# Performance work log

Measured on AMD Instinct MI355X. Metric: run time of the kernel, lower is better.

## Reference

```python
import jax, jax.numpy as jnp
import numpy as np
import math

B, S, D, H, L, K = 4, 2048, 256, 8, 2, 3  # batch, seq, dim, heads, MTA layers, conv kernel
HS = D // H
EPS = 1e-6


def layer_norm(x, g, b):
    m = jnp.mean(x, axis=-1, keepdims=True)
    v = jnp.mean((x - m) ** 2, axis=-1, keepdims=True)
    return (x - m) * jax.lax.rsqrt(v + EPS) * g + b


def temporal_encoder(x, W, b):
    # x: [B,S,D]; W: [L,K,D,D] (WIO), b: [L,D]. Stack of kernel-3 'SAME' Conv1d, GELU between.
    for i in range(L):
        x = jax.lax.conv_general_dilated(
            x, W[i], window_strides=(1,), padding=[(1, 1)],
            dimension_numbers=("NWC", "WIO", "NWC")) + b[i]
        if i < L - 1:
            x = jax.nn.gelu(x)
    return x


def setup_inputs() -> dict:
    key = jax.random.key(0)
    ks = jax.random.split(key, 10)
    w = lambda k, shape: jax.random.normal(k, shape, jnp.float32) * 0.02
    return {
        "x": jax.random.normal(ks[0], (B, S, D), jnp.float32),
        "ln1_g": jnp.ones((D,), jnp.float32), "ln1_b": jnp.zeros((D,), jnp.float32),
        "Wq": w(ks[1], (L, K, D, D)), "bq": jnp.zeros((L, D), jnp.float32),
        "Wk": w(ks[2], (L, K, D, D)), "bk": jnp.zeros((L, D), jnp.float32),
        "Wv": w(ks[3], (L, K, D, D)), "bv": jnp.zeros((L, D), jnp.float32),
        "ln2_g": jnp.ones((D,), jnp.float32), "ln2_b": jnp.zeros((D,), jnp.float32),
        "Wo1": w(ks[4], (D, D)), "bo1": jnp.zeros((D,), jnp.float32),
        "Wo2": w(ks[5], (D, D)), "bo2": jnp.zeros((D,), jnp.float32),
        "mask": jax.random.randint(ks[6], (B, S), 0, 2).astype(jnp.int32),
    }


def reference(x, ln1_g, ln1_b, Wq, bq, Wk, bk, Wv, bv, ln2_g, ln2_b, Wo1, bo1, Wo2, bo2, mask):
    b_, s_ = x.shape[0], x.shape[1]
    h = layer_norm(x, ln1_g, ln1_b)
    q = temporal_encoder(h, Wq, bq).reshape(b_, s_, H, HS)
    k = temporal_encoder(h, Wk, bk).reshape(b_, s_, H, HS)
    v = temporal_encoder(h, Wv, bv).reshape(b_, s_, H, HS)
    # attention scores [B,H,S,S]
    scores = jnp.einsum("bqhd,bkhd->bhqk", q, k) / math.sqrt(HS)
    m = mask[:, None, None, :].astype(scores.dtype)  # [B,1,1,S]
    scores = scores + (1.0 - m) * (-1e30)
    probs = jax.nn.softmax(scores, axis=-1)
    attn = jnp.einsum("bhqk,bkhd->bqhd", probs, v).reshape(b_, s_, D)
    residual = x + attn  # dropout p=0
    o = layer_norm(residual, ln2_g, ln2_b)
    o = jax.nn.gelu(o @ Wo1 + bo1)  # 1x1 Conv1D == per-token linear
    o = o @ Wo2 + bo2 + residual
    return o
```

## Files before the change

kernel.cpp:

```cpp
#include <hip/hip_runtime.h>
#include <hip/hip_bf16.h>
#include <math.h>

#define BB 4
#define SS 2048
#define DD 256
#define HH 8
#define HSZ 32

typedef __attribute__((ext_vector_type(8))) short short8;
typedef __attribute__((ext_vector_type(4))) float f32x4;

__device__ __forceinline__ void gload_lds16(const void* g, void* l) {
    __builtin_amdgcn_global_load_lds((const unsigned int*)g, (unsigned int*)l,
                                     16, 0, 0);
}

__device__ __forceinline__ float exp2_hw(float x) {
    float r;
    asm("v_exp_f32 %0, %1" : "=v"(r) : "v"(x));
    return r;
}

__device__ __forceinline__ unsigned int perm_pack(float a, float b, unsigned int sel) {
    unsigned int r;
    asm("v_perm_b32 %0, %1, %2, %3"
        : "=v"(r)
        : "v"(__float_as_uint(b)), "v"(__float_as_uint(a)), "s"(sel));
    return r;
}

__device__ __forceinline__ float gelu_f(float x) {
    float x3 = x * x * x;
    float z = 0.7978845608028654f * fmaf(0.044715f, x3, x);
    float e = __expf(2.0f * z);
    float t = 1.0f - 2.0f / (e + 1.0f);
    return 0.5f * x * (1.0f + t);
}

__device__ __forceinline__ unsigned short f2bf(float f) {
    unsigned int u = __float_as_uint(f);
    u = (u + 0x7fffu + ((u >> 16) & 1u)) >> 16;
    return (unsigned short)u;
}

template<bool HASRES>
__device__ __forceinline__ void ln_wave_body(
    int t, int lane,
    const float* __restrict__ x, const float* __restrict__ addin,
    const float* __restrict__ g, const float* __restrict__ bvec,
    float* __restrict__ resid_out, unsigned short* __restrict__ oln_bf)
{
    const int base = t * DD + lane * 4;
    float4 v4 = *(const float4*)&x[base];
    if (HASRES) {
        float4 a4 = *(const float4*)&addin[base];
        v4.x += a4.x; v4.y += a4.y; v4.z += a4.z; v4.w += a4.w;
        *(float4*)&resid_out[base] = v4;
    }
    float s = (v4.x + v4.y) + (v4.z + v4.w);
    #pragma unroll
    for (int o = 1; o < 64; o <<= 1) s += __shfl_xor(s, o);
    float mean = s * (1.0f / 256.0f);
    float dx = v4.x - mean, dy = v4.y - mean, dz = v4.z - mean, dw = v4.w - mean;
    float q = (dx * dx + dy * dy) + (dz * dz + dw * dw);
    #pragma unroll
    for (int o = 1; o < 64; o <<= 1) q += __shfl_xor(q, o);
    float r = rsqrtf(q * (1.0f / 256.0f) + 1e-6f);
    const float4 g4 = *(const float4*)&g[lane * 4];
    const float4 b4 = *(const float4*)&bvec[lane * 4];
    ushort4 o4;
    o4.x = f2bf(dx * r * g4.x + b4.x);
    o4.y = f2bf(dy * r * g4.y + b4.y);
    o4.z = f2bf(dz * r * g4.z + b4.z);
    o4.w = f2bf(dw * r * g4.w + b4.w);
    *(ushort4*)&oln_bf[base] = o4;
}

__global__ __launch_bounds__(256) void prep_kernel(
    const float* __restrict__ Wq, const float* __restrict__ Wk,
    const float* __restrict__ Wv, const float* __restrict__ Wo1,
    const float* __restrict__ Wo2, unsigned short* __restrict__ wt,
    const float* __restrict__ x, const float* __restrict__ ln1g,
    const float* __restrict__ ln1b, unsigned short* __restrict__ h_bf,
    const int* __restrict__ mask, float* __restrict__ maskf)
{
    if (blockIdx.x < 1280) {
        const int WCp = 3 * DD * DD;
        const int WMp = DD * DD;
        const float* src; unsigned short* dst; int rel;
        int i = blockIdx.x;
        if (i < 1152) {
            int seg = i / 192; rel = i % 192;
            src = seg == 0 ? Wq : seg == 1 ? Wq + WCp : seg == 2 ? Wk :
                  seg == 3 ? Wk + WCp : seg == 4 ? Wv : Wv + WCp;
            dst = wt + (size_t)seg * WCp;
        } else {
            int j = i - 1152; int seg = j / 64; rel = j % 64;
            src = seg == 0 ? Wo1 : Wo2;
            dst = wt + (size_t)6 * WCp + (size_t)seg * WMp;
        }
        __shared__ unsigned short t[32][33];
        const int tx = threadIdx.x & 31, ty = threadIdx.x >> 5;
        const int r0 = (rel / 8) * 32, c0 = (rel % 8) * 32;
        #pragma unroll
        for (int j = 0; j < 32; j += 8)
            t[ty + j][tx] = f2bf(src[(r0 + ty + j) * 256 + c0 + tx]);
        __syncthreads();
        #pragma unroll
        for (int j = 0; j < 32; j += 8) {
            unsigned int och = (unsigned int)(c0 + ty + j);
            unsigned int k   = (unsigned int)(r0 + tx);
            unsigned int u   = och * 32u + (k & 31u);
            u ^= ((u >> 6) & 7u) << 3;
            dst[(size_t)(k >> 5) * 8192 + u] = t[tx][ty + j];
        }
    } else if (blockIdx.x < 3328) {
        const int wv = threadIdx.x >> 6, lane = threadIdx.x & 63;
        ln_wave_body<false>((blockIdx.x - 1280) * 4 + wv, lane,
                            x, nullptr, ln1g, ln1b, nullptr, h_bf);
    } else {
        const float M_ON  = -8.0f * 1.4426950408889634f;
        const float M_OFF = -1.442695e30f;
        int i = (blockIdx.x - 3328) * 1024 + threadIdx.x * 4;
        int4 m4 = *(const int4*)&mask[i];
        float4 f4;
        f4.x = m4.x ? M_ON : M_OFF;
        f4.y = m4.y ? M_ON : M_OFF;
        f4.z = m4.z ? M_ON : M_OFF;
        f4.w = m4.w ? M_ON : M_OFF;
        *(float4*)&maskf[i] = f4;
    }
}

__global__ __launch_bounds__(256, 3) void convdual_kernel(
    const unsigned short* __restrict__ in,
    const unsigned short* __restrict__ W0a, const unsigned short* __restrict__ W0b,
    const unsigned short* __restrict__ W0c,
    const unsigned short* __restrict__ W1a, const unsigned short* __restrict__ W1b,
    const unsigned short* __restrict__ W1c,
    const float* __restrict__ ba, const float* __restrict__ bb,
    const float* __restrict__ bc,
    unsigned short* __restrict__ oQ, unsigned short* __restrict__ oK,
    unsigned short* __restrict__ oV, int S)
{
    constexpr int LDW = 264;
    __shared__ __align__(16) unsigned short stage[36 * LDW];
    __shared__ __align__(16) unsigned short wbuf[2][8192];

    unsigned short* const inter = stage;

    const int set = blockIdx.x % 3;
    const int tile = blockIdx.x / 3;
    const unsigned short* W0 = set == 0 ? W0a : (set == 1 ? W0b : W0c);
    const unsigned short* W1 = set == 0 ? W1a : (set == 1 ? W1b : W1c);
    const float* bias         = set == 0 ? ba  : (set == 1 ? bb  : bc);
    unsigned short* outp      = set == 0 ? oQ  : (set == 1 ? oK  : oV);

    const int tid = threadIdx.x;
    const int lane = tid & 63, wv = tid >> 6;
    const int lm = lane & 15, lq = lane >> 4;
    const int tpb = S / 32;
    const int b = tile / tpb;
    const int s0 = (tile % tpb) * 32;
    const int NC = S / 32;
    const int c = s0 >> 5;

    for (int i = tid; i < 36 * 32; i += 256) {
        int r = i >> 5, c8 = (i & 31) << 3;
        int s = s0 + r - 2;
        int4 val = make_int4(0, 0, 0, 0);
        if (s >= 0 && s < S)
            val = *(const int4*)&in[(size_t)(b * S + s) * 256 + c8];
        *(int4*)&stage[r * LDW + c8] = val;
    }

    const int n0 = wv * 64;

    const int wq = wv * 4096;
    const char* w0p = (const char*)W0 + wq + lane * 16;
    const char* w1p = (const char*)W1 + wq + lane * 16;
    char* const wb0 = (char*)wbuf;

    unsigned int boff[4];
    #pragma unroll
    for (int nt = 0; nt < 4; ++nt) {
        unsigned int och = (unsigned int)(n0 + nt * 16 + lm);
        unsigned int R = och * 64u + (unsigned int)lq * 16u;
        boff[nt] = R ^ (((R >> 7) & 7u) << 4);
    }

    __syncthreads();

    {
        f32x4 acc[3][4];
        #pragma unroll
        for (int mt = 0; mt < 3; ++mt)
            #pragma unroll
            for (int nt = 0; nt < 4; ++nt) acc[mt][nt] = (f32x4){0.f, 0.f, 0.f, 0.f};

        #pragma unroll
        for (int j = 0; j < 4; ++j) gload_lds16(w0p + j * 1024,         wb0 + wq + j * 1024);
        #pragma unroll
        for (int j = 0; j < 4; ++j) gload_lds16(w0p + 16384 + j * 1024, wb0 + 16384 + wq + j * 1024);

        short8 a0c, a1c, a2c;
        {
            const int icc0 = lq * 8;
            int r20 = 32 + lm; r20 = r20 > 35 ? 35 : r20;
            a0c = *(const short8*)&stage[lm * LDW + icc0];
            a1c = *(const short8*)&stage[(16 + lm) * LDW + icc0];
            a2c = *(const short8*)&stage[r20 * LDW + icc0];
        }

        asm volatile("s_waitcnt vmcnt(4)" ::: "memory");
        __builtin_amdgcn_sched_barrier(0);
        short8 bfc[4];
        #pragma unroll
        for (int nt = 0; nt < 4; ++nt)
            bfc[nt] = *(const short8*)(wb0 + boff[nt]);

        #pragma unroll
        for (int it = 0; it < 24; ++it) {
            asm volatile("s_waitcnt lgkmcnt(0)" ::: "memory");
            __builtin_amdgcn_sched_barrier(0);
            if (it + 2 < 24) {
                char* ld = wb0 + ((it & 1) << 14) + wq;
                const int soff = (it + 2) * 16384;
                #pragma unroll
                for (int j = 0; j < 4; ++j)
                    gload_lds16(w0p + soff + j * 1024, ld + j * 1024);
            }
            __builtin_amdgcn_sched_barrier(0);
            if (it < 22)       { asm volatile("s_waitcnt vmcnt(4)" ::: "memory"); }
            else if (it == 22) { asm volatile("s_waitcnt vmcnt(0)" ::: "memory"); }
            __builtin_amdgcn_sched_barrier(0);

            short8 bfn[4];
            short8 a0n, a1n, a2n;
            if (it + 1 < 24) {
                const char* wb = wb0 + (((it + 1) & 1) << 14);
                #pragma unroll
                for (int nt = 0; nt < 4; ++nt)
                    bfn[nt] = *(const short8*)(wb + boff[nt]);
                const int kk = (it + 1) >> 3;
                const int icc = ((it + 1) & 7) * 32 + lq * 8;
                int r2 = kk + 32 + lm; r2 = r2 > 35 ? 35 : r2;
                a0n = *(const short8*)&stage[(kk + lm) * LDW + icc];
                a1n = *(const short8*)&stage[(kk + 16 + lm) * LDW + icc];
                a2n = *(const short8*)&stage[r2 * LDW + icc];
            }
            __builtin_amdgcn_s_setprio(1);
            #pragma unroll
            for (int nt = 0; nt < 4; ++nt) {
                acc[0][nt] = __builtin_amdgcn_mfma_f32_16x16x32_bf16(a0c, bfc[nt], acc[0][nt], 0, 0, 0);
                acc[1][nt] = __builtin_amdgcn_mfma_f32_16x16x32_bf16(a1c, bfc[nt], acc[1][nt], 0, 0, 0);
                acc[2][nt] = __builtin_amdgcn_mfma_f32_16x16x32_bf16(a2c, bfc[nt], acc[2][nt], 0, 0, 0);
            }
            __builtin_amdgcn_s_setprio(0);
            if (it + 1 < 24) {
                #pragma unroll
                for (int nt = 0; nt < 4; ++nt) bfc[nt] = bfn[nt];
                a0c = a0n; a1c = a1n; a2c = a2n;
            }
        }

        __syncthreads();

        #pragma unroll
        for (int j = 0; j < 4; ++j) gload_lds16(w1p + j * 1024,         wb0 + wq + j * 1024);
        #pragma unroll
        for (int j = 0; j < 4; ++j) gload_lds16(w1p + 16384 + j * 1024, wb0 + 16384 + wq + j * 1024);

        #pragma unroll
        for (int mt = 0; mt < 3; ++mt)
            #pragma unroll
            for (int nt = 0; nt < 4; ++nt) {
                int ch = n0 + nt * 16 + lm;
                float bv = bias[ch];
                #pragma unroll
                for (int r = 0; r < 4; ++r) {
                    int j = mt * 16 + lq * 4 + r;
                    if (j < 34) {
                        int token = s0 - 1 + j;
                        unsigned short v = (token >= 0 && token < S)
                            ? f2bf(gelu_f(acc[mt][nt][r] + bv)) : (unsigned short)0;
                        inter[j * LDW + ch] = v;
                    }
                }
            }
    }
    __syncthreads();

    f32x4 acc2[2][4];
    #pragma unroll
    for (int mt = 0; mt < 2; ++mt)
        #pragma unroll
        for (int nt = 0; nt < 4; ++nt) acc2[mt][nt] = (f32x4){0.f, 0.f, 0.f, 0.f};
    {
        char* const wb0 = (char*)wbuf;
        short8 a0c, a1c;
        {
            const int icc0 = lq * 8;
            a0c = *(const short8*)&inter[lm * LDW + icc0];
            a1c = *(const short8*)&inter[(16 + lm) * LDW + icc0];
        }

        asm volatile("s_waitcnt vmcnt(4)" ::: "memory");
        __builtin_amdgcn_sched_barrier(0);
        short8 bfc[4];
        #pragma unroll
        for (int nt = 0; nt < 4; ++nt)
            bfc[nt] = *(const short8*)(wb0 + boff[nt]);

        #pragma unroll
        for (int it = 0; it < 24; ++it) {
            asm volatile("s_waitcnt lgkmcnt(0)" ::: "memory");
            __builtin_amdgcn_sched_barrier(0);
            if (it + 2 < 24) {
                char* ld = wb0 + ((it & 1) << 14) + wq;
                const int soff = (it + 2) * 16384;
                #pragma unroll
                for (int j = 0; j < 4; ++j)
                    gload_lds16(w1p + soff + j * 1024, ld + j * 1024);
            }
            __builtin_amdgcn_sched_barrier(0);
            if (it < 22)       { asm volatile("s_waitcnt vmcnt(4)" ::: "memory"); }
            else if (it == 22) { asm volatile("s_waitcnt vmcnt(0)" ::: "memory"); }
            __builtin_amdgcn_sched_barrier(0);

            short8 bfn[4];
            short8 a0n, a1n;
            if (it + 1 < 24) {
                const char* wb = wb0 + (((it + 1) & 1) << 14);
                #pragma unroll
                for (int nt = 0; nt < 4; ++nt)
                    bfn[nt] = *(const short8*)(wb + boff[nt]);
                const int kk = (it + 1) >> 3;
                const int icc = ((it + 1) & 7) * 32 + lq * 8;
                a0n = *(const short8*)&inter[(kk + lm) * LDW + icc];
                a1n = *(const short8*)&inter[(kk + 16 + lm) * LDW + icc];
            }
            __builtin_amdgcn_s_setprio(1);
            #pragma unroll
            for (int nt = 0; nt < 4; ++nt) {
                acc2[0][nt] = __builtin_amdgcn_mfma_f32_16x16x32_bf16(a0c, bfc[nt], acc2[0][nt], 0, 0, 0);
                acc2[1][nt] = __builtin_amdgcn_mfma_f32_16x16x32_bf16(a1c, bfc[nt], acc2[1][nt], 0, 0, 0);
            }
            __builtin_amdgcn_s_setprio(0);
            if (it + 1 < 24) {
                #pragma unroll
                for (int nt = 0; nt < 4; ++nt) bfc[nt] = bfn[nt];
                a0c = a0n; a1c = a1n;
            }
        }
    }

    __syncthreads();
    if (set < 2) {
        #pragma unroll
        for (int mt = 0; mt < 2; ++mt)
            #pragma unroll
            for (int nt = 0; nt < 4; ++nt) {
                int o = n0 + nt * 16 + lm;
                int d = o & 31, h = o >> 5;
                float bv = bias[256 + o];
                #pragma unroll
                for (int r = 0; r < 4; ++r) {
                    int t = lq * 4 + r;
                    stage[mt * 4096 + (h * 64 + (d >> 3) * 16 + t) * 8 + (d & 7)] =
                        f2bf(acc2[mt][nt][r] + bv);
                }
            }
        __syncthreads();
        int h = tid >> 5;
        size_t base = ((size_t)(b * 8 + h) * NC + c) * 1024;
        #pragma unroll
        for (int half = 0; half < 2; ++half) {
            int4 v0 = *(const int4*)&stage[half * 4096 + tid * 16];
            int4 v1 = *(const int4*)&stage[half * 4096 + tid * 16 + 8];
            size_t dst = base + half * 512 + (tid & 31) * 16;
            *(int4*)&outp[dst] = v0;
            *(int4*)&outp[dst + 8] = v1;
        }
    } else {
        #pragma unroll
        for (int mt = 0; mt < 2; ++mt)
            #pragma unroll
            for (int nt = 0; nt < 4; ++nt) {
                int o = n0 + nt * 16 + lm;
                int d = o & 31, h = o >> 5;
                float bv = bias[256 + o];
                #pragma unroll
                for (int r = 0; r < 4; ++r) {
                    int t = lq * 4 + r;
                    stage[mt * 4096 +
                          ((h * 2 + (d >> 4)) * 32 + (t >> 3) * 16 + (d & 15)) * 8 + (t & 7)] =
                        f2bf(acc2[mt][nt][r] + bv);
                }
            }
        __syncthreads();
        int h = tid >> 5, dh = (tid >> 4) & 1;
        size_t base = ((size_t)(b * 8 + h) * NC + c) * 1024;
        #pragma unroll
        for (int half = 0; half < 2; ++half) {
            int4 v0 = *(const int4*)&stage[half * 4096 + tid * 16];
            int4 v1 = *(const int4*)&stage[half * 4096 + tid * 16 + 8];
            size_t dst = base + dh * 512 + half * 256 + (tid & 15) * 16;
            *(int4*)&outp[dst] = v0;
            *(int4*)&outp[dst + 8] = v1;
        }
    }
}

__global__ __launch_bounds__(256, 2) void tail_kernel(
    const float* __restrict__ x, const float* __restrict__ attn,
    const float* __restrict__ g2, const float* __restrict__ b2,
    const unsigned short* __restrict__ W1, const float* __restrict__ bo1,
    const unsigned short* __restrict__ W2, const float* __restrict__ bo2,
    float* __restrict__ out, int S)
{
    constexpr int LDW = 264;
    __shared__ __align__(16) unsigned short h_lds[16 * LDW];
    __shared__ __align__(16) unsigned short h2_lds[16 * LDW];
    __shared__ __align__(16) float resid_lds[16][DD];
    __shared__ __align__(16) unsigned short wbuf[2][8192];

    const int tid = threadIdx.x;
    const int lane = tid & 63, wv = tid >> 6;
    const int lm = lane & 15, lq = lane >> 4;
    const int t0 = blockIdx.x * 16;
    const int n0 = wv * 64;

    const int wq = wv * 4096;
    const char* w1p = (const char*)W1 + wq + lane * 16;
    const char* w2p = (const char*)W2 + wq + lane * 16;
    char* const wb0 = (char*)wbuf;

    unsigned int boff[4];
    #pragma unroll
    for (int nt = 0; nt < 4; ++nt) {
        unsigned int och = (unsigned int)(n0 + nt * 16 + lm);
        unsigned int R = och * 64u + (unsigned int)lq * 16u;
        boff[nt] = R ^ (((R >> 7) & 7u) << 4);
    }

    #pragma unroll
    for (int j = 0; j < 4; ++j) gload_lds16(w1p + j * 1024,         wb0 + wq + j * 1024);
    #pragma unroll
    for (int j = 0; j < 4; ++j) gload_lds16(w1p + 16384 + j * 1024, wb0 + 16384 + wq + j * 1024);

    #pragma unroll
    for (int j = 0; j < 4; ++j) {
        int t = wv * 4 + j;
        int base = (t0 + t) * DD + lane * 4;
        float4 v4 = *(const float4*)&x[base];
        float4 a4 = *(const float4*)&attn[base];
        v4.x += a4.x; v4.y += a4.y; v4.z += a4.z; v4.w += a4.w;
        *(float4*)&resid_lds[t][lane * 4] = v4;
        float s = (v4.x + v4.y) + (v4.z + v4.w);
        #pragma unroll
        for (int o = 1; o < 64; o <<= 1) s += __shfl_xor(s, o);
        float mean = s * (1.0f / 256.0f);
        float dx = v4.x - mean, dy = v4.y - mean, dz = v4.z - mean, dw = v4.w - mean;
        float q = (dx * dx + dy * dy) + (dz * dz + dw * dw);
        #pragma unroll
        for (int o = 1; o < 64; o <<= 1) q += __shfl_xor(q, o);
        float r = rsqrtf(q * (1.0f / 256.0f) + 1e-6f);
        const float4 g4 = *(const float4*)&g2[lane * 4];
        const float4 b4 = *(const float4*)&b2[lane * 4];
        ushort4 o4;
        o4.x = f2bf(dx * r * g4.x + b4.x);
        o4.y = f2bf(dy * r * g4.y + b4.y);
        o4.z = f2bf(dz * r * g4.z + b4.z);
        o4.w = f2bf(dw * r * g4.w + b4.w);
        *(ushort4*)&h_lds[t * LDW + lane * 4] = o4;
    }
    __syncthreads();

    {
        f32x4 acc[4];
        #pragma unroll
        for (int nt = 0; nt < 4; ++nt) acc[nt] = (f32x4){0.f, 0.f, 0.f, 0.f};

        short8 a0c = *(const short8*)&h_lds[lm * LDW + lq * 8];
        asm volatile("s_waitcnt vmcnt(4)" ::: "memory");
        __builtin_amdgcn_sched_barrier(0);
        short8 bfc[4];
        #pragma unroll
        for (int nt = 0; nt < 4; ++nt)
            bfc[nt] = *(const short8*)(wb0 + boff[nt]);

        #pragma unroll
        for (int it = 0; it < 8; ++it) {
            asm volatile("s_waitcnt lgkmcnt(0)" ::: "memory");
            __builtin_amdgcn_sched_barrier(0);
            if (it + 2 < 8) {
                char* ld = wb0 + ((it & 1) << 14) + wq;
                const int soff = (it + 2) * 16384;
                #pragma unroll
                for (int j = 0; j < 4; ++j)
                    gload_lds16(w1p + soff + j * 1024, ld + j * 1024);
            }
            __builtin_amdgcn_sched_barrier(0);
            if (it < 6)       { asm volatile("s_waitcnt vmcnt(4)" ::: "memory"); }
            else if (it == 6) { asm volatile("s_waitcnt vmcnt(0)" ::: "memory"); }
            __builtin_amdgcn_sched_barrier(0);

            short8 bfn[4], a0n;
            if (it + 1 < 8) {
                const char* wb = wb0 + (((it + 1) & 1) << 14);
                #pragma unroll
                for (int nt = 0; nt < 4; ++nt)
                    bfn[nt] = *(const short8*)(wb + boff[nt]);
                a0n = *(const short8*)&h_lds[lm * LDW + (it + 1) * 32 + lq * 8];
            }
            __builtin_amdgcn_s_setprio(1);
            #pragma unroll
            for (int nt = 0; nt < 4; ++nt)
                acc[nt] = __builtin_amdgcn_mfma_f32_16x16x32_bf16(a0c, bfc[nt], acc[nt], 0, 0, 0);
            __builtin_amdgcn_s_setprio(0);
            if (it + 1 < 8) {
                #pragma unroll
                for (int nt = 0; nt < 4; ++nt) bfc[nt] = bfn[nt];
                a0c = a0n;
            }
        }

        asm volatile("s_waitcnt lgkmcnt(0)" ::: "memory");
        __builtin_amdgcn_sched_barrier(0);
        #pragma unroll
        for (int j = 0; j < 4; ++j) gload_lds16(w2p + j * 1024,         wb0 + wq + j * 1024);
        #pragma unroll
        for (int j = 0; j < 4; ++j) gload_lds16(w2p + 16384 + j * 1024, wb0 + 16384 + wq + j * 1024);

        #pragma unroll
        for (int nt = 0; nt < 4; ++nt) {
            int ch = n0 + nt * 16 + lm;
            float bv = bo1[ch];
            #pragma unroll
            for (int r = 0; r < 4; ++r) {
                int tok = lq * 4 + r;
                h2_lds[tok * LDW + ch] = f2bf(gelu_f(acc[nt][r] + bv));
            }
        }
    }
    __syncthreads();

    {
        f32x4 acc[4];
        #pragma unroll
        for (int nt = 0; nt < 4; ++nt) acc[nt] = (f32x4){0.f, 0.f, 0.f, 0.f};

        short8 a0c = *(const short8*)&h2_lds[lm * LDW + lq * 8];
        asm volatile("s_waitcnt vmcnt(4)" ::: "memory");
        __builtin_amdgcn_sched_barrier(0);
        short8 bfc[4];
        #pragma unroll
        for (int nt = 0; nt < 4; ++nt)
            bfc[nt] = *(const short8*)(wb0 + boff[nt]);

        #pragma unroll
        for (int it = 0; it < 8; ++it) {
            asm volatile("s_waitcnt lgkmcnt(0)" ::: "memory");
            __builtin_amdgcn_sched_barrier(0);
            if (it + 2 < 8) {
                char* ld = wb0 + ((it & 1) << 14) + wq;
                const int soff = (it + 2) * 16384;
                #pragma unroll
                for (int j = 0; j < 4; ++j)
                    gload_lds16(w2p + soff + j * 1024, ld + j * 1024);
            }
            __builtin_amdgcn_sched_barrier(0);
            if (it < 6)       { asm volatile("s_waitcnt vmcnt(4)" ::: "memory"); }
            else if (it == 6) { asm volatile("s_waitcnt vmcnt(0)" ::: "memory"); }
            __builtin_amdgcn_sched_barrier(0);

            short8 bfn[4], a0n;
            if (it + 1 < 8) {
                const char* wb = wb0 + (((it + 1) & 1) << 14);
                #pragma unroll
                for (int nt = 0; nt < 4; ++nt)
                    bfn[nt] = *(const short8*)(wb + boff[nt]);
                a0n = *(const short8*)&h2_lds[lm * LDW + (it + 1) * 32 + lq * 8];
            }
            __builtin_amdgcn_s_setprio(1);
            #pragma unroll
            for (int nt = 0; nt < 4; ++nt)
                acc[nt] = __builtin_amdgcn_mfma_f32_16x16x32_bf16(a0c, bfc[nt], acc[nt], 0, 0, 0);
            __builtin_amdgcn_s_setprio(0);
            if (it + 1 < 8) {
                #pragma unroll
                for (int nt = 0; nt < 4; ++nt) bfc[nt] = bfn[nt];
                a0c = a0n;
            }
        }
        #pragma unroll
        for (int nt = 0; nt < 4; ++nt) {
            int ch = n0 + nt * 16 + lm;
            float bv = bo2[ch];
            #pragma unroll
            for (int r = 0; r < 4; ++r) {
                int tok = lq * 4 + r;
                out[(size_t)(t0 + tok) * DD + ch] = acc[nt][r] + bv + resid_lds[tok][ch];
            }
        }
    }
}

__global__ __launch_bounds__(256) void attn_mfma_kernel(
    const unsigned short* __restrict__ Qf, const unsigned short* __restrict__ Kf,
    const unsigned short* __restrict__ Vf, const float* __restrict__ maskf,
    float* __restrict__ Out, int S, int H)
{
    constexpr int LDP = 40;
    __shared__ __align__(16) unsigned short p_lds[4][16 * LDP];

    const int bh = ((blockIdx.x & 7) << 2) | ((blockIdx.x >> 3) & 3);
    const int qt = (blockIdx.x >> 5) * 64;
    const int b = bh / H;
    const int tid = threadIdx.x;
    const int lane = tid & 63, wv = tid >> 6;
    const int lm = lane & 15, lq = lane >> 4;
    const int q0 = qt + wv * 16;
    const int NC = S / 32;

    const size_t base = (size_t)bh * NC * 1024;
    short8 qfrag = *(const short8*)&Qf[base + (size_t)(q0 >> 5) * 1024
                                      + ((q0 >> 4) & 1) * 512 + lane * 8];
    const unsigned short* kp = Kf + base + lane * 8;
    const unsigned short* vp = Vf + base + lane * 8;

    short8 ones;
    #pragma unroll
    for (int j = 0; j < 8; ++j) ones[j] = (short)0x3F80;

    f32x4 o0 = {0.f, 0.f, 0.f, 0.f}, o1 = {0.f, 0.f, 0.f, 0.f};
    const f32x4 zf = {0.f, 0.f, 0.f, 0.f};
    float l[4] = {0.f, 0.f, 0.f, 0.f};

    const float scale2 = 0.17677669529663687f * 1.4426950408889634f;
    const unsigned int psel = 0x07060302u;
    const float* mp0 = maskf + b * S + lq * 4;
    const float* mp1 = mp0 + 16;

    unsigned short* pw = p_lds[wv];
    const int pst = lm * LDP + lq * 4;
    const int prd = lm * LDP + lq * 8;

    short8 k0c = *(const short8*)(kp);
    short8 k1c = *(const short8*)(kp + 512);
    short8 v0c = *(const short8*)(vp);
    short8 v1c = *(const short8*)(vp + 512);

    #pragma unroll 2
    for (int c = 0; c < NC; ++c) {
        int cn = c + 1 < NC ? c + 1 : c;
        short8 k0n = *(const short8*)(kp + (size_t)cn * 1024);
        short8 k1n = *(const short8*)(kp + (size_t)cn * 1024 + 512);
        short8 v0n = *(const short8*)(vp + (size_t)cn * 1024);
        short8 v1n = *(const short8*)(vp + (size_t)cn * 1024 + 512);

        f32x4 s0 = __builtin_amdgcn_mfma_f32_16x16x32_bf16(k0c, qfrag, zf, 0, 0, 0);
        f32x4 s1 = __builtin_amdgcn_mfma_f32_16x16x32_bf16(k1c, qfrag, zf, 0, 0, 0);

        float4 mf0 = *(const float4*)(mp0 + c * 32);
        float4 mf1 = *(const float4*)(mp1 + c * 32);

        float p[8];
        p[0] = exp2_hw(fmaf(s0[0], scale2, mf0.x));
        p[1] = exp2_hw(fmaf(s0[1], scale2, mf0.y));
        p[2] = exp2_hw(fmaf(s0[2], scale2, mf0.z));
        p[3] = exp2_hw(fmaf(s0[3], scale2, mf0.w));
        p[4] = exp2_hw(fmaf(s1[0], scale2, mf1.x));
        p[5] = exp2_hw(fmaf(s1[1], scale2, mf1.y));
        p[6] = exp2_hw(fmaf(s1[2], scale2, mf1.z));
        p[7] = exp2_hw(fmaf(s1[3], scale2, mf1.w));

        uint2 w0, w1;
        w0.x = perm_pack(p[0], p[1], psel); w0.y = perm_pack(p[2], p[3], psel);
        w1.x = perm_pack(p[4], p[5], psel); w1.y = perm_pack(p[6], p[7], psel);
        *(uint2*)&pw[pst] = w0;
        *(uint2*)&pw[pst + 16] = w1;

        short8 pA = *(const short8*)&pw[prd];

        f32x4 lf = __builtin_amdgcn_mfma_f32_16x16x32_bf16(pA, ones, zf, 0, 0, 0);
        o0 = __builtin_amdgcn_mfma_f32_16x16x32_bf16(pA, v0c, o0, 0, 0, 0);
        o1 = __builtin_amdgcn_mfma_f32_16x16x32_bf16(pA, v1c, o1, 0, 0, 0);
        #pragma unroll
        for (int r = 0; r < 4; ++r) l[r] += lf[r];

        k0c = k0n; k1c = k1n; v0c = v0n; v1c = v1n;
    }

    #pragma unroll
    for (int r = 0; r < 4; ++r) {
        float inv = 1.0f / l[r];
        size_t ob = (size_t)(b * S + q0 + lq * 4 + r) * 256 + (bh % H) * 32;
        Out[ob + lm] = o0[r] * inv;
        Out[ob + 16 + lm] = o1[r] * inv;
    }
}

extern "C" void kernel_launch(void* const* d_in, const int* in_sizes, int n_in,
                              void* d_out, int out_size, void* d_ws, size_t ws_size,
                              hipStream_t stream) {
    (void)in_sizes; (void)n_in; (void)out_size; (void)ws_size;
    const float* x    = (const float*)d_in[0];
    const float* ln1g = (const float*)d_in[1];
    const float* ln1b = (const float*)d_in[2];
    const float* Wq   = (const float*)d_in[3];
    const float* bq   = (const float*)d_in[4];
    const float* Wk   = (const float*)d_in[5];
    const float* bk   = (const float*)d_in[6];
    const float* Wv   = (const float*)d_in[7];
    const float* bv   = (const float*)d_in[8];
    const float* ln2g = (const float*)d_in[9];
    const float* ln2b = (const float*)d_in[10];
    const float* Wo1  = (const float*)d_in[11];
    const float* bo1  = (const float*)d_in[12];
    const float* Wo2  = (const float*)d_in[13];
    const float* bo2  = (const float*)d_in[14];
    const int*   mask = (const int*)d_in[15];
    float* out = (float*)d_out;

    const int S = SS, H = HH;
    const int T = BB * SS;
    const size_t NE = (size_t)T * DD;
    float* ws    = (float*)d_ws;
    float* attn  = ws + 0 * NE;
    float* maskf = ws + 1 * NE;
    unsigned short* qf_g  = (unsigned short*)(ws + 2 * NE);
    unsigned short* kf_g  = qf_g + NE;
    unsigned short* h_bf  = kf_g + NE;
    unsigned short* wt    = h_bf + NE;
    const int WC = 3 * DD * DD;
    const int WM = DD * DD;
    unsigned short* wtq0 = wt;
    unsigned short* wtq1 = wt + WC;
    unsigned short* wtk0 = wt + 2 * WC;
    unsigned short* wtk1 = wt + 3 * WC;
    unsigned short* wtv0 = wt + 4 * WC;
    unsigned short* wtv1 = wt + 5 * WC;
    unsigned short* wto1 = wt + 6 * WC;
    unsigned short* wto2 = wt + 6 * WC + WM;
    unsigned short* vf_g = wt + 6 * WC + 2 * WM;

    prep_kernel<<<1280 + T / 4 + 8, 256, 0, stream>>>(
        Wq, Wk, Wv, Wo1, Wo2, wt, x, ln1g, ln1b, h_bf, mask, maskf);

    convdual_kernel<<<(T / 32) * 3, 256, 0, stream>>>(
        h_bf, wtq0, wtk0, wtv0, wtq1, wtk1, wtv1, bq, bk, bv,
        qf_g, kf_g, vf_g, S);

    attn_mfma_kernel<<<BB * H * (S / 64), 256, 0, stream>>>(qf_g, kf_g, vf_g, maskf, attn, S, H);

    tail_kernel<<<T / 16, 256, 0, stream>>>(
        x, attn, ln2g, ln2b, wto1, bo1, wto2, bo2, out, S);
}
```

Before: 189.5 us.

## Software-pipeline attention loop with double-buffered P tile in LDS

```diff
diff --git a/kernel.cpp b/kernel.cpp
--- a/kernel.cpp
+++ b/kernel.cpp
@@ -614,7 +614,7 @@
     float* __restrict__ Out, int S, int H)
 {
     constexpr int LDP = 40;
-    __shared__ __align__(16) unsigned short p_lds[4][16 * LDP];
+    __shared__ __align__(16) unsigned short p_lds[4][2][16 * LDP];
 
     const int bh = ((blockIdx.x & 7) << 2) | ((blockIdx.x >> 3) & 3);
     const int qt = (blockIdx.x >> 5) * 64;
@@ -636,37 +636,28 @@
     for (int j = 0; j < 8; ++j) ones[j] = (short)0x3F80;
 
     f32x4 o0 = {0.f, 0.f, 0.f, 0.f}, o1 = {0.f, 0.f, 0.f, 0.f};
+    f32x4 lacc = {0.f, 0.f, 0.f, 0.f};
     const f32x4 zf = {0.f, 0.f, 0.f, 0.f};
-    float l[4] = {0.f, 0.f, 0.f, 0.f};
 
     const float scale2 = 0.17677669529663687f * 1.4426950408889634f;
     const unsigned int psel = 0x07060302u;
     const float* mp0 = maskf + b * S + lq * 4;
     const float* mp1 = mp0 + 16;
 
-    unsigned short* pw = p_lds[wv];
+    unsigned short* pwb[2] = { p_lds[wv][0], p_lds[wv][1] };
     const int pst = lm * LDP + lq * 4;
     const int prd = lm * LDP + lq * 8;
 
     short8 k0c = *(const short8*)(kp);
     short8 k1c = *(const short8*)(kp + 512);
-    short8 v0c = *(const short8*)(vp);
-    short8 v1c = *(const short8*)(vp + 512);
-
-    #pragma unroll 2
-    for (int c = 0; c < NC; ++c) {
-        int cn = c + 1 < NC ? c + 1 : c;
-        short8 k0n = *(const short8*)(kp + (size_t)cn * 1024);
-        short8 k1n = *(const short8*)(kp + (size_t)cn * 1024 + 512);
-        short8 v0n = *(const short8*)(vp + (size_t)cn * 1024);
-        short8 v1n = *(const short8*)(vp + (size_t)cn * 1024 + 512);
-
+    short8 v0p = *(const short8*)(vp);
+    short8 v1p = *(const short8*)(vp + 512);
+
+    {
         f32x4 s0 = __builtin_amdgcn_mfma_f32_16x16x32_bf16(k0c, qfrag, zf, 0, 0, 0);
         f32x4 s1 = __builtin_amdgcn_mfma_f32_16x16x32_bf16(k1c, qfrag, zf, 0, 0, 0);
-
-        float4 mf0 = *(const float4*)(mp0 + c * 32);
-        float4 mf1 = *(const float4*)(mp1 + c * 32);
-
+        float4 mf0 = *(const float4*)(mp0);
+        float4 mf1 = *(const float4*)(mp1);
         float p[8];
         p[0] = exp2_hw(fmaf(s0[0], scale2, mf0.x));
         p[1] = exp2_hw(fmaf(s0[1], scale2, mf0.y));
@@ -676,27 +667,62 @@
         p[5] = exp2_hw(fmaf(s1[1], scale2, mf1.y));
         p[6] = exp2_hw(fmaf(s1[2], scale2, mf1.z));
         p[7] = exp2_hw(fmaf(s1[3], scale2, mf1.w));
-
         uint2 w0, w1;
         w0.x = perm_pack(p[0], p[1], psel); w0.y = perm_pack(p[2], p[3], psel);
         w1.x = perm_pack(p[4], p[5], psel); w1.y = perm_pack(p[6], p[7], psel);
-        *(uint2*)&pw[pst] = w0;
-        *(uint2*)&pw[pst + 16] = w1;
-
-        short8 pA = *(const short8*)&pw[prd];
-
-        f32x4 lf = __builtin_amdgcn_mfma_f32_16x16x32_bf16(pA, ones, zf, 0, 0, 0);
-        o0 = __builtin_amdgcn_mfma_f32_16x16x32_bf16(pA, v0c, o0, 0, 0, 0);
-        o1 = __builtin_amdgcn_mfma_f32_16x16x32_bf16(pA, v1c, o1, 0, 0, 0);
-        #pragma unroll
-        for (int r = 0; r < 4; ++r) l[r] += lf[r];
-
-        k0c = k0n; k1c = k1n; v0c = v0n; v1c = v1n;
+        *(uint2*)&pwb[0][pst] = w0;
+        *(uint2*)&pwb[0][pst + 16] = w1;
+    }
+
+    k0c = *(const short8*)(kp + 1024);
+    k1c = *(const short8*)(kp + 1024 + 512);
+
+    #pragma unroll 2
+    for (int c = 1; c < NC; ++c) {
+        int cn = c + 1 < NC ? c + 1 : c;
+        short8 v0n = *(const short8*)(vp + (size_t)c * 1024);
+        short8 v1n = *(const short8*)(vp + (size_t)c * 1024 + 512);
+        short8 k0n = *(const short8*)(kp + (size_t)cn * 1024);
+        short8 k1n = *(const short8*)(kp + (size_t)cn * 1024 + 512);
+
+        f32x4 s0 = __builtin_amdgcn_mfma_f32_16x16x32_bf16(k0c, qfrag, zf, 0, 0, 0);
+        f32x4 s1 = __builtin_amdgcn_mfma_f32_16x16x32_bf16(k1c, qfrag, zf, 0, 0, 0);
+
+        short8 pA = *(const short8*)&pwb[(c - 1) & 1][prd];
+        lacc = __builtin_amdgcn_mfma_f32_16x16x32_bf16(pA, ones, lacc, 0, 0, 0);
+        o0   = __builtin_amdgcn_mfma_f32_16x16x32_bf16(pA, v0p, o0, 0, 0, 0);
+        o1   = __builtin_amdgcn_mfma_f32_16x16x32_bf16(pA, v1p, o1, 0, 0, 0);
+
+        float4 mf0 = *(const float4*)(mp0 + c * 32);
+        float4 mf1 = *(const float4*)(mp1 + c * 32);
+        float p[8];
+        p[0] = exp2_hw(fmaf(s0[0], scale2, mf0.x));
+        p[1] = exp2_hw(fmaf(s0[1], scale2, mf0.y));
+        p[2] = exp2_hw(fmaf(s0[2], scale2, mf0.z));
+        p[3] = exp2_hw(fmaf(s0[3], scale2, mf0.w));
+        p[4] = exp2_hw(fmaf(s1[0], scale2, mf1.x));
+        p[5] = exp2_hw(fmaf(s1[1], scale2, mf1.y));
+        p[6] = exp2_hw(fmaf(s1[2], scale2, mf1.z));
+        p[7] = exp2_hw(fmaf(s1[3], scale2, mf1.w));
+        uint2 w0, w1;
+        w0.x = perm_pack(p[0], p[1], psel); w0.y = perm_pack(p[2], p[3], psel);
+        w1.x = perm_pack(p[4], p[5], psel); w1.y = perm_pack(p[6], p[7], psel);
+        *(uint2*)&pwb[c & 1][pst] = w0;
+        *(uint2*)&pwb[c & 1][pst + 16] = w1;
+
+        v0p = v0n; v1p = v1n; k0c = k0n; k1c = k1n;
+    }
+
+    {
+        short8 pA = *(const short8*)&pwb[(NC - 1) & 1][prd];
+        lacc = __builtin_amdgcn_mfma_f32_16x16x32_bf16(pA, ones, lacc, 0, 0, 0);
+        o0   = __builtin_amdgcn_mfma_f32_16x16x32_bf16(pA, v0p, o0, 0, 0, 0);
+        o1   = __builtin_amdgcn_mfma_f32_16x16x32_bf16(pA, v1p, o1, 0, 0, 0);
     }
 
     #pragma unroll
     for (int r = 0; r < 4; ++r) {
-        float inv = 1.0f / l[r];
+        float inv = 1.0f / lacc[r];
         size_t ob = (size_t)(b * S + q0 + lq * 4 + r) * 256 + (bh % H) * 32;
         Out[ob + lm] = o0[r] * inv;
         Out[ob + 16 + lm] = o1[r] * inv;
```

Measured after the change: 208.9 us. 10.3% more time.
